# Kernel optimization log

Hardware: AMD Instinct MI355X
Metric: run time of the kernel (lower is better)

The kernel has to match this reference:

```python
import jax, jax.numpy as jnp
import numpy as np

G, K, N, T = 16, 2048, 2048, 16384  # groups, in_features, out_features, total_tokens


def setup_inputs() -> dict:
    key = jax.random.key(0)
    k1, k2 = jax.random.split(key)
    hidden_states = jax.random.normal(k1, (T, K), dtype=jnp.float32)
    # kaiming_uniform_(a=sqrt(5)) on [G, K, N] -> bound = sqrt(6 / ((1 + 5) * fan_in)) = 1/sqrt(K)
    bound = 1.0 / np.sqrt(K)
    weight = jax.random.uniform(k2, (G, K, N), dtype=jnp.float32, minval=-bound, maxval=bound)
    tokens_per_group = T // G
    tokens_per_expert = jnp.full((G,), tokens_per_group, dtype=jnp.int32)
    # offsets[0] = 0, offsets[i] = start of group i (matches _group_sizes_from_offsets)
    offsets = jnp.arange(G, dtype=jnp.int32) * tokens_per_group
    blockscale_offsets = offsets  # unused by the eager math path; carried for signature fidelity
    return {
        "hidden_states": hidden_states,
        "weight": weight,
        "offsets": offsets,
        "blockscale_offsets": blockscale_offsets,
        "tokens_per_expert": tokens_per_expert,
    }


def reference(hidden_states, weight, offsets, blockscale_offsets, tokens_per_expert):
    # Grouped (ragged) GEMM: rows [offsets[g] : offsets[g]+tokens_per_expert[g]] of
    # hidden_states are multiplied by weight[g] ([K, N]). tokens_per_expert equals the
    # group sizes derived from offsets in the torch module's eager fallback.
    # jax.lax.ragged_dot is the exact grouped-mm primitive (no dense [T,K,N] gather).
    return jax.lax.ragged_dot(hidden_states, weight, tokens_per_expert)
```

## Files before the change

kernel.cpp:

```cpp
#include <hip/hip_runtime.h>
#include <cstdint>
#include <cstddef>

#define GRP 16
#define KD  2048
#define ND  2048
#define TD  16384

#define BM 128
#define BN 128
#define BK 32

typedef __bf16 bf16x8 __attribute__((ext_vector_type(8)));
typedef float  f32x4  __attribute__((ext_vector_type(4)));

__device__ __forceinline__ uint16_t f2bf(float f) {
  uint32_t u = __builtin_bit_cast(uint32_t, f);
  u += 0x7fffu + ((u >> 16) & 1u);
  return (uint16_t)(u >> 16);
}

__device__ __forceinline__ void gload16(const void* g, void* l) {
  __builtin_amdgcn_global_load_lds((__attribute__((address_space(1))) void*)g,
                                   (__attribute__((address_space(3))) void*)l,
                                   16, 0, 0);
}

__device__ __forceinline__ int find_group(const int* tokens, int row0) {
  int g = GRP - 1, start = 0;
  for (int i = 0; i < GRP; ++i) {
    int sz = tokens[i];
    if (row0 < start + sz) { g = i; break; }
    start += sz;
  }
  return g;
}

__global__ __launch_bounds__(256) void h2bf_kernel(const float* __restrict__ in,
                                                   uint16_t* __restrict__ out) {
  const size_t idx = ((size_t)blockIdx.x * 256 + threadIdx.x) * 8;
  const float4 a = *(const float4*)(in + idx);
  const float4 b = *(const float4*)(in + idx + 4);
  uint4 p;
  p.x = (uint32_t)f2bf(a.x) | ((uint32_t)f2bf(a.y) << 16);
  p.y = (uint32_t)f2bf(a.z) | ((uint32_t)f2bf(a.w) << 16);
  p.z = (uint32_t)f2bf(b.x) | ((uint32_t)f2bf(b.y) << 16);
  p.w = (uint32_t)f2bf(b.z) | ((uint32_t)f2bf(b.w) << 16);
  *(uint4*)(out + idx) = p;
}

__global__ __launch_bounds__(256) void wtrans_kernel(const float* __restrict__ w,
                                                     uint16_t* __restrict__ wT) {
  __shared__ uint32_t tile[64][33];
  const int g  = blockIdx.z;
  const int n0 = blockIdx.x * 64;
  const int k0 = blockIdx.y * 64;
  const float* src = w + (size_t)g * KD * ND;
  uint16_t* dst = wT + (size_t)g * ND * KD;
  const int t = threadIdx.x;

  {
    const int kl = t >> 4;
    const int n4 = (t & 15) * 4;
    uint16_t* t16 = (uint16_t*)&tile[0][0];
    for (int kk = 0; kk < 4; ++kk) {
      const int k = kk * 16 + kl;
      const float4 v = *(const float4*)(src + (size_t)(k0 + k) * ND + n0 + n4);
      t16[(n4 + 0) * 66 + k] = f2bf(v.x);
      t16[(n4 + 1) * 66 + k] = f2bf(v.y);
      t16[(n4 + 2) * 66 + k] = f2bf(v.z);
      t16[(n4 + 3) * 66 + k] = f2bf(v.w);
    }
  }
  __syncthreads();
  {
    const int n  = t >> 2;
    const int kq = (t & 3) * 8;
    uint32_t v[8];
    for (int j = 0; j < 8; ++j) v[j] = tile[n][kq + j];
    uint32_t* o = (uint32_t*)(dst + (size_t)(n0 + n) * KD + k0) + kq;
    *(uint4*)(o + 0) = make_uint4(v[0], v[1], v[2], v[3]);
    *(uint4*)(o + 4) = make_uint4(v[4], v[5], v[6], v[7]);
  }
}

__global__ __launch_bounds__(256) void gemm_kernel(const uint16_t* __restrict__ A,
                                                   const uint16_t* __restrict__ Bt,
                                                   const int* __restrict__ tokens,
                                                   float* __restrict__ C) {
  __shared__ uint16_t Alds[BM * BK];
  __shared__ uint16_t Blds[BN * BK];

  const int t    = threadIdx.x;
  const int n0   = blockIdx.x * BN;
  const int row0 = blockIdx.y * BM;

  const int g = find_group(tokens, row0);
  const uint16_t* Bg = Bt + (size_t)g * ND * KD;

  const int lane = t & 63;
  const int wid  = t >> 6;
  const int wm   = wid & 1;
  const int wn   = wid >> 1;
  const int l16  = lane & 15;
  const int quad = lane >> 4;

  f32x4 acc[4][4] = {};

  const int c1 = t, c2 = t + 256;
  const int r1 = c1 >> 2, ko1 = (c1 & 3) * 8;
  const int r2 = c2 >> 2, ko2 = (c2 & 3) * 8;
  const uint16_t* Ap1 = A  + (size_t)(row0 + r1) * KD + ko1;
  const uint16_t* Ap2 = A  + (size_t)(row0 + r2) * KD + ko2;
  const uint16_t* Bp1 = Bg + (size_t)(n0  + r1) * KD + ko1;
  const uint16_t* Bp2 = Bg + (size_t)(n0  + r2) * KD + ko2;
  uint16_t* Al1 = &Alds[c1 * 8];
  uint16_t* Al2 = &Alds[c2 * 8];
  uint16_t* Bl1 = &Blds[c1 * 8];
  uint16_t* Bl2 = &Blds[c2 * 8];

  for (int k0 = 0; k0 < KD; k0 += BK) {
    __syncthreads();
    gload16(Ap1 + k0, Al1);
    gload16(Ap2 + k0, Al2);
    gload16(Bp1 + k0, Bl1);
    gload16(Bp2 + k0, Bl2);
    __syncthreads();

    bf16x8 af[4], bfr[4];
    for (int mi = 0; mi < 4; ++mi)
      af[mi] = *(const bf16x8*)&Alds[(wm * 64 + mi * 16 + l16) * BK + quad * 8];
    for (int ni = 0; ni < 4; ++ni)
      bfr[ni] = *(const bf16x8*)&Blds[(wn * 64 + ni * 16 + l16) * BK + quad * 8];

    for (int mi = 0; mi < 4; ++mi)
      for (int ni = 0; ni < 4; ++ni)
        acc[mi][ni] = __builtin_amdgcn_mfma_f32_16x16x32_bf16(af[mi], bfr[ni],
                                                              acc[mi][ni], 0, 0, 0);
  }

  for (int mi = 0; mi < 4; ++mi) {
    const int m = row0 + wm * 64 + mi * 16 + quad * 4;
    for (int ni = 0; ni < 4; ++ni) {
      const int n = n0 + wn * 64 + ni * 16 + l16;
      for (int r = 0; r < 4; ++r)
        C[(size_t)(m + r) * ND + n] = acc[mi][ni][r];
    }
  }
}

__global__ __launch_bounds__(256) void fb_gemm(const float* __restrict__ A,
                                               const float* __restrict__ W,
                                               const int* __restrict__ tokens,
                                               float* __restrict__ C) {
  __shared__ float As[16][64];
  __shared__ float Bs[16][65];
  const int n0 = blockIdx.x * 64;
  const int m0 = blockIdx.y * 64;
  const int g = find_group(tokens, m0);
  const float* Wg = W + (size_t)g * KD * ND;
  const int tx = threadIdx.x & 15, ty = threadIdx.x >> 4;
  float acc[4][4] = {};
  for (int k0 = 0; k0 < KD; k0 += 16) {
    for (int e = threadIdx.x; e < 64 * 16; e += 256) {
      int m = e >> 4, k = e & 15;
      As[k][m] = A[(size_t)(m0 + m) * KD + k0 + k];
    }
    for (int e = threadIdx.x; e < 64 * 16; e += 256) {
      int n = e & 63, k = e >> 6;
      Bs[k][n] = Wg[(size_t)(k0 + k) * ND + n0 + n];
    }
    __syncthreads();
    for (int k = 0; k < 16; ++k)
      for (int i = 0; i < 4; ++i)
        for (int j = 0; j < 4; ++j)
          acc[i][j] += As[k][ty * 4 + i] * Bs[k][tx * 4 + j];
    __syncthreads();
  }
  for (int i = 0; i < 4; ++i)
    for (int j = 0; j < 4; ++j)
      C[(size_t)(m0 + ty * 4 + i) * ND + n0 + tx * 4 + j] = acc[i][j];
}

extern "C" void kernel_launch(void* const* d_in, const int* in_sizes, int n_in,
                              void* d_out, int out_size, void* d_ws, size_t ws_size,
                              hipStream_t stream) {
  const float* hidden = (const float*)d_in[0];
  const float* weight = (const float*)d_in[1];
  const int*   tokens = (const int*)d_in[4];
  float* out = (float*)d_out;

  const size_t needA = (size_t)TD * KD * 2;
  const size_t needB = (size_t)GRP * ND * KD * 2;

  if (ws_size >= needA + needB) {
    uint16_t* hB = (uint16_t*)d_ws;
    uint16_t* wT = (uint16_t*)((char*)d_ws + needA);
    h2bf_kernel<<<(int)(((size_t)TD * KD) / (256 * 8)), 256, 0, stream>>>(hidden, hB);
    wtrans_kernel<<<dim3(ND / 64, KD / 64, GRP), 256, 0, stream>>>(weight, wT);
    gemm_kernel<<<dim3(ND / BN, TD / BM), 256, 0, stream>>>(hB, wT, tokens, out);
  } else {
    fb_gemm<<<dim3(ND / 64, TD / 64), 256, 0, stream>>>(hidden, weight, tokens, out);
  }
}
```

Measured before the change: 734.1 us.

## Double GEMM K-tile to 64 with XOR-swizzled LDS layout; vectorize weight transpose

```diff
diff --git a/kernel.cpp b/kernel.cpp
--- a/kernel.cpp
+++ b/kernel.cpp
@@ -9,7 +9,7 @@
 
 #define BM 128
 #define BN 128
-#define BK 32
+#define BK 64
 
 typedef __bf16 bf16x8 __attribute__((ext_vector_type(8)));
 typedef float  f32x4  __attribute__((ext_vector_type(4)));
@@ -60,27 +60,28 @@
   const int t = threadIdx.x;
 
   {
-    const int kl = t >> 4;
+    const int k2 = t >> 4;
     const int n4 = (t & 15) * 4;
-    uint16_t* t16 = (uint16_t*)&tile[0][0];
-    for (int kk = 0; kk < 4; ++kk) {
-      const int k = kk * 16 + kl;
-      const float4 v = *(const float4*)(src + (size_t)(k0 + k) * ND + n0 + n4);
-      t16[(n4 + 0) * 66 + k] = f2bf(v.x);
-      t16[(n4 + 1) * 66 + k] = f2bf(v.y);
-      t16[(n4 + 2) * 66 + k] = f2bf(v.z);
-      t16[(n4 + 3) * 66 + k] = f2bf(v.w);
+    for (int half = 0; half < 2; ++half) {
+      const int kp = half * 16 + k2;
+      const int k  = kp * 2;
+      const float4 v0 = *(const float4*)(src + (size_t)(k0 + k)     * ND + n0 + n4);
+      const float4 v1 = *(const float4*)(src + (size_t)(k0 + k + 1) * ND + n0 + n4);
+      tile[n4 + 0][kp] = (uint32_t)f2bf(v0.x) | ((uint32_t)f2bf(v1.x) << 16);
+      tile[n4 + 1][kp] = (uint32_t)f2bf(v0.y) | ((uint32_t)f2bf(v1.y) << 16);
+      tile[n4 + 2][kp] = (uint32_t)f2bf(v0.z) | ((uint32_t)f2bf(v1.z) << 16);
+      tile[n4 + 3][kp] = (uint32_t)f2bf(v0.w) | ((uint32_t)f2bf(v1.w) << 16);
     }
   }
   __syncthreads();
   {
     const int n  = t >> 2;
     const int kq = (t & 3) * 8;
-    uint32_t v[8];
-    for (int j = 0; j < 8; ++j) v[j] = tile[n][kq + j];
+    const uint4 a = *(const uint4*)&tile[n][kq];
+    const uint4 b = *(const uint4*)&tile[n][kq + 4];
     uint32_t* o = (uint32_t*)(dst + (size_t)(n0 + n) * KD + k0) + kq;
-    *(uint4*)(o + 0) = make_uint4(v[0], v[1], v[2], v[3]);
-    *(uint4*)(o + 4) = make_uint4(v[4], v[5], v[6], v[7]);
+    *(uint4*)(o + 0) = a;
+    *(uint4*)(o + 4) = b;
   }
 }
 
@@ -107,36 +108,45 @@
 
   f32x4 acc[4][4] = {};
 
-  const int c1 = t, c2 = t + 256;
-  const int r1 = c1 >> 2, ko1 = (c1 & 3) * 8;
-  const int r2 = c2 >> 2, ko2 = (c2 & 3) * 8;
-  const uint16_t* Ap1 = A  + (size_t)(row0 + r1) * KD + ko1;
-  const uint16_t* Ap2 = A  + (size_t)(row0 + r2) * KD + ko2;
-  const uint16_t* Bp1 = Bg + (size_t)(n0  + r1) * KD + ko1;
-  const uint16_t* Bp2 = Bg + (size_t)(n0  + r2) * KD + ko2;
-  uint16_t* Al1 = &Alds[c1 * 8];
-  uint16_t* Al2 = &Alds[c2 * 8];
-  uint16_t* Bl1 = &Blds[c1 * 8];
-  uint16_t* Bl2 = &Blds[c2 * 8];
+  const uint16_t* Apt[4]; const uint16_t* Bpt[4];
+  uint16_t *Al[4], *Bl[4];
+  for (int i = 0; i < 4; ++i) {
+    const int c = t + 256 * i;
+    const int r = c >> 3;
+    const int ko = ((c & 7) ^ (r & 7)) * 8;
+    Apt[i] = A  + (size_t)(row0 + r) * KD + ko;
+    Bpt[i] = Bg + (size_t)(n0  + r) * KD + ko;
+    Al[i] = &Alds[c * 8];
+    Bl[i] = &Blds[c * 8];
+  }
+
+  int aoff[2][4], boff[2][4];
+  for (int h = 0; h < 2; ++h) {
+    for (int mi = 0; mi < 4; ++mi) {
+      const int r = wm * 64 + mi * 16 + l16;
+      aoff[h][mi] = r * BK + (((h * 4 + quad) ^ (r & 7)) * 8);
+    }
+    for (int ni = 0; ni < 4; ++ni) {
+      const int r = wn * 64 + ni * 16 + l16;
+      boff[h][ni] = r * BK + (((h * 4 + quad) ^ (r & 7)) * 8);
+    }
+  }
 
   for (int k0 = 0; k0 < KD; k0 += BK) {
     __syncthreads();
-    gload16(Ap1 + k0, Al1);
-    gload16(Ap2 + k0, Al2);
-    gload16(Bp1 + k0, Bl1);
-    gload16(Bp2 + k0, Bl2);
-    __syncthreads();
-
-    bf16x8 af[4], bfr[4];
-    for (int mi = 0; mi < 4; ++mi)
-      af[mi] = *(const bf16x8*)&Alds[(wm * 64 + mi * 16 + l16) * BK + quad * 8];
-    for (int ni = 0; ni < 4; ++ni)
-      bfr[ni] = *(const bf16x8*)&Blds[(wn * 64 + ni * 16 + l16) * BK + quad * 8];
-
-    for (int mi = 0; mi < 4; ++mi)
-      for (int ni = 0; ni < 4; ++ni)
-        acc[mi][ni] = __builtin_amdgcn_mfma_f32_16x16x32_bf16(af[mi], bfr[ni],
-                                                              acc[mi][ni], 0, 0, 0);
+    for (int i = 0; i < 4; ++i) gload16(Apt[i] + k0, Al[i]);
+    for (int i = 0; i < 4; ++i) gload16(Bpt[i] + k0, Bl[i]);
+    __syncthreads();
+
+    for (int h = 0; h < 2; ++h) {
+      bf16x8 af[4], bfr[4];
+      for (int mi = 0; mi < 4; ++mi) af[mi]  = *(const bf16x8*)&Alds[aoff[h][mi]];
+      for (int ni = 0; ni < 4; ++ni) bfr[ni] = *(const bf16x8*)&Blds[boff[h][ni]];
+      for (int mi = 0; mi < 4; ++mi)
+        for (int ni = 0; ni < 4; ++ni)
+          acc[mi][ni] = __builtin_amdgcn_mfma_f32_16x16x32_bf16(af[mi], bfr[ni],
+                                                                acc[mi][ni], 0, 0, 0);
+    }
   }
 
   for (int mi = 0; mi < 4; ++mi) {
```

After: 676.0 us. -7.9%, faster.
